# Performance work log

Hardware: AMD Instinct MI355X
Metric: run time of the kernel (lower is better)

## Reference

```python
import jax, jax.numpy as jnp
import numpy as np

NUM_HEADS = 12
HEAD_CH = 64
WINDOW = 4


def _relative_to_absolute(x):
    # x: (B, H, L, 2L-1) -> (B, H, L, L) via skew trick
    B, H, L, _ = x.shape
    x = jnp.pad(x, ((0, 0), (0, 0), (0, 0), (0, 1)))        # (B,H,L,2L)
    x = x.reshape(B, H, L * 2 * L)
    x = jnp.pad(x, ((0, 0), (0, 0), (0, L - 1)))
    x = x.reshape(B, H, L + 1, 2 * L - 1)
    return x[:, :, :L, L - 1:]


def _get_relative_embeddings(emb, L):
    # emb: (H, 2W+1, D) -> (H, 2L-1, D)
    pad = max(0, L - WINDOW - 1)
    start = max(0, WINDOW - L + 1)
    e = jnp.pad(emb, ((0, 0), (pad, pad), (0, 0)))
    return e[:, start:start + 2 * L - 1, :]


def _forward(x, wq, bq, wk, bk, wv, bv, wo, bo, emb_rel_k, emb_rel_v):
    B, C, L = x.shape
    H, D = NUM_HEADS, HEAD_CH
    scale = 1.0 / np.sqrt(D).astype(np.float32)

    # 1x1 conv == channel matmul
    q = jnp.einsum('oc,bcl->bol', wq, x) + bq[None, :, None]
    k = jnp.einsum('oc,bcl->bol', wk, x) + bk[None, :, None]
    v = jnp.einsum('oc,bcl->bol', wv, x) + bv[None, :, None]

    # (B, C, L) -> (B, H, L, D)
    q = q.reshape(B, H, D, L).transpose(0, 1, 3, 2)
    k = k.reshape(B, H, D, L).transpose(0, 1, 3, 2)
    v = v.reshape(B, H, D, L).transpose(0, 1, 3, 2)

    score = jnp.einsum('bhld,bhmd->bhlm', q, k) * scale      # (B,H,L,L)

    rel_k = _get_relative_embeddings(emb_rel_k, L)           # (H, 2L-1, D)
    s_rel = jnp.einsum('bhld,hmd->bhlm', q, rel_k)           # (B,H,L,2L-1)
    score = score + _relative_to_absolute(s_rel) * scale

    attn = jax.nn.softmax(score, axis=-1)                    # dropout p=0 -> identity

    res = jnp.einsum('bhlm,bhmd->bhld', attn, v)             # (B,H,L,D)

    # absolute_to_relative skew
    a = jnp.pad(attn, ((0, 0), (0, 0), (0, 0), (0, L - 1)))
    a = a.reshape(B, H, L * (2 * L - 1))
    a = jnp.pad(a, ((0, 0), (0, 0), (L, 0)))
    rel_w = a.reshape(B, H, L, 2 * L)[:, :, :, 1:]           # (B,H,L,2L-1)

    rel_v = _get_relative_embeddings(emb_rel_v, L)           # (H, 2L-1, D)
    res = res + jnp.einsum('bhlm,hmd->bhld', rel_w, rel_v)

    res = res.transpose(0, 1, 3, 2).reshape(B, H * D, L)     # (B, C, L)
    out = jnp.einsum('oc,bcl->bol', wo, res) + bo[None, :, None]
    return out


def setup_inputs() -> dict:
    key = jax.random.key(0)
    ks = jax.random.split(key, 11)
    B, C, L = 4, 768, 1024
    rel_std = HEAD_CH ** (-0.5)
    xavier = np.sqrt(6.0 / (C + C)).astype(np.float32)
    return {
        'x': jax.random.normal(ks[0], (B, C, L), jnp.float32),
        'wq': jax.random.uniform(ks[1], (C, C), jnp.float32, -xavier, xavier),
        'bq': jnp.zeros((C,), jnp.float32),
        'wk': jax.random.uniform(ks[2], (C, C), jnp.float32, -xavier, xavier),
        'bk': jnp.zeros((C,), jnp.float32),
        'wv': jax.random.uniform(ks[3], (C, C), jnp.float32, -xavier, xavier),
        'bv': jnp.zeros((C,), jnp.float32),
        'wo': jax.random.normal(ks[4], (C, C), jnp.float32) * 0.02,
        'bo': jnp.zeros((C,), jnp.float32),
        'emb_rel_k': jax.random.normal(ks[5], (NUM_HEADS, 2 * WINDOW + 1, HEAD_CH), jnp.float32) * rel_std,
        'emb_rel_v': jax.random.normal(ks[6], (NUM_HEADS, 2 * WINDOW + 1, HEAD_CH), jnp.float32) * rel_std,
    }


def reference(x, wq, bq, wk, bk, wv, bv, wo, bo, emb_rel_k, emb_rel_v):
    return _forward(x, wq, bq, wk, bk, wv, bv, wo, bo, emb_rel_k, emb_rel_v)
```

## Files before the change

kernel.cpp:

```cpp
#include <hip/hip_runtime.h>

#define NB   4
#define NH   12
#define HD   64
#define CCH  768
#define LQ   1024
#define SCALE 0.125f
#define STAB  4.0f
#define SC2  0.18033688f
#define ST2  5.7707802f
#define WELE (CCH*CCH)

typedef unsigned short u16;
typedef __bf16 bf16x8 __attribute__((ext_vector_type(8)));
typedef unsigned short u16x8 __attribute__((ext_vector_type(8)));
typedef unsigned short u16x4 __attribute__((ext_vector_type(4)));
typedef float floatx4 __attribute__((ext_vector_type(4)));

__device__ __forceinline__ float bf2f(u16 u) {
    union { unsigned int i; float f; } x; x.i = ((unsigned int)u) << 16; return x.f;
}
__device__ __forceinline__ u16 f2bf_u(float f) {
    union { float f; unsigned int i; } x; x.f = f;
    unsigned int i = x.i;
    return (u16)((i + 0x7FFFu + ((i >> 16) & 1u)) >> 16);
}
__device__ __forceinline__ void glds16(const u16* g, u16* l) {
    __builtin_amdgcn_global_load_lds(
        (const __attribute__((address_space(1))) unsigned int*)g,
        (__attribute__((address_space(3))) unsigned int*)l, 16, 0, 0);
}

__global__ __launch_bounds__(256) void convert_w_kernel(
    const float* __restrict__ wq, const float* __restrict__ wk,
    const float* __restrict__ wv, const float* __restrict__ wo,
    u16* __restrict__ wb)
{
    const int p = blockIdx.y;
    const float* src = (p == 0) ? wq : (p == 1) ? wk : (p == 2) ? wv : wo;
    u16* dst = wb + (size_t)p * WELE;
    const int idx = (blockIdx.x * 256 + threadIdx.x) * 4;
    const float4 v = *reinterpret_cast<const float4*>(src + idx);
    u16x4 o;
    o[0] = f2bf_u(v.x); o[1] = f2bf_u(v.y); o[2] = f2bf_u(v.z); o[3] = f2bf_u(v.w);
    *reinterpret_cast<u16x4*>(dst + idx) = o;
}

__global__ __launch_bounds__(256) void transpose_x_kernel(
    const float* __restrict__ x, u16* __restrict__ xT)
{
    __shared__ u16 tile[64 * 68];
    const int l0 = blockIdx.x * 64, c0 = blockIdx.y * 64, b = blockIdx.z;
    const int t = threadIdx.x;
    const float* xb = x + (size_t)b * CCH * LQ;
    {
        const int l = t & 63, cg = t >> 6;
        for (int i = 0; i < 16; ++i) {
            const int c = cg * 16 + i;
            tile[c * 68 + l] = f2bf_u(xb[(size_t)(c0 + c) * LQ + l0 + l]);
        }
    }
    __syncthreads();
    {
        const int c = t & 63, lg = t >> 6;
        for (int i = 0; i < 16; ++i) {
            const int l = lg * 16 + i;
            xT[((size_t)b * LQ + l0 + l) * CCH + c0 + c] = tile[c * 68 + l];
        }
    }
}

#define GEMM_CORE(Ag, Bg)                                                     \
    __shared__ __align__(16) u16 a_tile[128 * 64];                            \
    __shared__ __align__(16) u16 b_tile[128 * 64];                            \
    const int t = threadIdx.x;                                                \
    const int wave = t >> 6, lane = t & 63;                                   \
    const int quad = lane >> 4, l16 = lane & 15;                              \
    const int wm = (wave >> 1) * 64, wn = (wave & 1) * 64;                    \
    floatx4 acc[4][4];                                                        \
    _Pragma("unroll") for (int mi = 0; mi < 4; ++mi)                          \
        _Pragma("unroll") for (int ni = 0; ni < 4; ++ni)                      \
            _Pragma("unroll") for (int r = 0; r < 4; ++r) acc[mi][ni][r] = 0.f;\
    for (int k0 = 0; k0 < CCH; k0 += 64) {                                    \
        __syncthreads();                                                      \
        _Pragma("unroll") for (int i = 0; i < 4; ++i) {                       \
            const int sbase = wave * 256 + i * 64;                            \
            const int s = sbase + lane;                                       \
            const int m = s >> 3, pos = s & 7;                                \
            const int gpos = pos ^ (m & 7);                                   \
            glds16(Ag + (size_t)(m0 + m) * CCH + k0 + gpos * 8,               \
                   &a_tile[sbase * 8]);                                       \
            glds16(Bg + (size_t)(n0 + m) * CCH + k0 + gpos * 8,               \
                   &b_tile[sbase * 8]);                                       \
        }                                                                     \
        __syncthreads();                                                      \
        bf16x8 af[2][4], bfr[2][4];                                           \
        _Pragma("unroll") for (int s = 0; s < 2; ++s)                         \
            _Pragma("unroll") for (int i = 0; i < 4; ++i) {                   \
                const int am = wm + i * 16 + l16;                             \
                const int bn = wn + i * 16 + l16;                             \
                const int c = s * 4 + quad;                                   \
                af[s][i]  = *reinterpret_cast<const bf16x8*>(                 \
                    &a_tile[(am * 8 + (c ^ (am & 7))) * 8]);                  \
                bfr[s][i] = *reinterpret_cast<const bf16x8*>(                 \
                    &b_tile[(bn * 8 + (c ^ (bn & 7))) * 8]);                  \
            }                                                                 \
        _Pragma("unroll") for (int s = 0; s < 2; ++s)                         \
            _Pragma("unroll") for (int mi = 0; mi < 4; ++mi)                  \
                _Pragma("unroll") for (int ni = 0; ni < 4; ++ni)              \
                    acc[mi][ni] = __builtin_amdgcn_mfma_f32_16x16x32_bf16(    \
                        af[s][mi], bfr[s][ni], acc[mi][ni], 0, 0, 0);         \
    }

__global__ __launch_bounds__(256) void proj_qkv_kernel(
    const u16* __restrict__ xT, const u16* __restrict__ wb,
    const float* __restrict__ bq, const float* __restrict__ bk,
    const float* __restrict__ bv,
    u16* __restrict__ Qw, u16* __restrict__ Kw, u16* __restrict__ Vw)
{
    const int z = blockIdx.z, b = z / 3, p = z % 3;
    int m0, n0;
    const u16 *Ag, *Bg;
    if (p == 1) {
        m0 = blockIdx.x * 128;
        n0 = blockIdx.y * 128;
        Ag = xT + (size_t)b * LQ * CCH;
        Bg = wb + (size_t)WELE;
    } else {
        n0 = blockIdx.x * 128;
        m0 = blockIdx.y * 128;
        Ag = wb + (size_t)p * WELE;
        Bg = xT + (size_t)b * LQ * CCH;
    }

    GEMM_CORE(Ag, Bg)

    if (p == 1) {
        u16* Y = Kw + (size_t)b * LQ * CCH;
#pragma unroll
        for (int mi = 0; mi < 4; ++mi) {
#pragma unroll
            for (int r = 0; r < 4; ++r) {
                const int l = m0 + wm + mi * 16 + quad * 4 + r;
#pragma unroll
                for (int ni = 0; ni < 4; ++ni) {
                    const int o = n0 + wn + ni * 16 + l16;
                    Y[(size_t)l * CCH + o] = f2bf_u(acc[mi][ni][r] + bk[o]);
                }
            }
        }
    } else {
        const float* bias = (p == 0) ? bq : bv;
        u16* Y = ((p == 0) ? Qw : Vw) + (size_t)b * CCH * LQ;
#pragma unroll
        for (int mi = 0; mi < 4; ++mi) {
#pragma unroll
            for (int r = 0; r < 4; ++r) {
                const int o = m0 + wm + mi * 16 + quad * 4 + r;
                const float bb = bias[o];
#pragma unroll
                for (int ni = 0; ni < 4; ++ni) {
                    const int l = n0 + wn + ni * 16 + l16;
                    Y[(size_t)o * LQ + l] = f2bf_u(acc[mi][ni][r] + bb);
                }
            }
        }
    }
}

__global__ __launch_bounds__(256) void proj_out_kernel(
    const u16* __restrict__ resb, const u16* __restrict__ wb,
    const float* __restrict__ bo, float* __restrict__ out)
{
    const int b = blockIdx.z;
    const int n0 = blockIdx.x * 128, m0 = blockIdx.y * 128;
    const u16* Ag = wb + (size_t)3 * WELE;
    const u16* Bg = resb + (size_t)b * LQ * CCH;
    float* Y = out + (size_t)b * CCH * LQ;

    GEMM_CORE(Ag, Bg)

#pragma unroll
    for (int mi = 0; mi < 4; ++mi) {
#pragma unroll
        for (int r = 0; r < 4; ++r) {
            const int o = m0 + wm + mi * 16 + quad * 4 + r;
            const float bb = bo[o];
#pragma unroll
            for (int ni = 0; ni < 4; ++ni) {
                const int l = n0 + wn + ni * 16 + l16;
                Y[(size_t)o * LQ + l] = acc[mi][ni][r] + bb;
            }
        }
    }
}

#define KSTRIDE 72
#define TILE_E  (64 * 64)

__device__ __forceinline__ void stage_kv(
    const u16* __restrict__ Kb, const u16* __restrict__ Vb, int j0,
    u16* kb_lds, u16* vb_lds, int wave, int lane)
{
#pragma unroll
    for (int i = 0; i < 4; ++i) {
        const int sidx = wave * 4 + i;
        if (sidx < 8) {
            const int sbase = sidx * 64;
            const int s = sbase + lane;
            const int m = s >> 3, pos = s & 7;
            const int gpos = pos ^ (m & 7);
            glds16(Kb + (size_t)(j0 + m) * CCH + gpos * 8, &kb_lds[sbase * 8]);
        } else {
            const int sbase = (sidx - 8) * 64;
            const int s = sbase + lane;
            const int m = s >> 3, pos = s & 7;
            const int gpos = pos ^ (m & 7);
            glds16(Vb + (size_t)m * LQ + j0 + gpos * 8, &vb_lds[sbase * 8]);
        }
    }
}

__global__ __launch_bounds__(256) void attn_kernel(
    const u16* __restrict__ Qw, const u16* __restrict__ Kt,
    const u16* __restrict__ Vw,
    const float* __restrict__ erk, const float* __restrict__ erv,
    u16* __restrict__ resb)
{
    __shared__ __align__(16) u16 kbuf[2 * TILE_E];
    __shared__ __align__(16) u16 vbuf[2 * TILE_E];
    __shared__ __align__(16) u16 p_lds[4 * 16 * KSTRIDE];
    __shared__ float bias_lds[64 * 9];
    __shared__ float bandw_lds[64 * 9];
    __shared__ float erk_lds[9 * 64];
    __shared__ float erv_lds[9 * 64];

    const int t = threadIdx.x;
    const int wave = t >> 6, lane = t & 63;
    const int quad = lane >> 4, l16 = lane & 15;
    const int l0 = blockIdx.x * 64, h = blockIdx.y, b = blockIdx.z;
    const int rbase = wave * 16;
    const size_t base = ((size_t)b * CCH + (size_t)h * HD) * LQ;
    const u16* Qb = Qw + base;
    const u16* Vb = Vw + base;
    const u16* Kb = Kt + (size_t)b * LQ * CCH + (size_t)h * HD;

    for (int i = t; i < 9 * 64; i += 256) {
        erk_lds[i] = erk[(size_t)h * 9 * 64 + i];
        erv_lds[i] = erv[(size_t)h * 9 * 64 + i];
    }

    bf16x8 qa0, qa1;
    {
        const int lg = l0 + rbase + l16;
        union { u16x8 u; bf16x8 v; } t0, t1;
#pragma unroll
        for (int jj = 0; jj < 8; ++jj) {
            t0.u[jj] = Qb[(size_t)(quad * 8 + jj) * LQ + lg];
            t1.u[jj] = Qb[(size_t)(32 + quad * 8 + jj) * LQ + lg];
        }
        qa0 = t0.v; qa1 = t1.v;
    }

    stage_kv(Kb, Vb, 0, kbuf, vbuf, wave, lane);

    __syncthreads();

    {
        union { bf16x8 v; u16x8 u; } a0, a1; a0.v = qa0; a1.v = qa1;
        float qf[16];
#pragma unroll
        for (int jj = 0; jj < 8; ++jj) { qf[jj] = bf2f(a0.u[jj]); qf[8 + jj] = bf2f(a1.u[jj]); }
        for (int dl = 0; dl < 9; ++dl) {
            float s = 0.f;
#pragma unroll
            for (int jj = 0; jj < 8; ++jj) {
                s += qf[jj]     * erk_lds[dl * 64 + quad * 8 + jj];
                s += qf[8 + jj] * erk_lds[dl * 64 + 32 + quad * 8 + jj];
            }
            s += __shfl_xor(s, 16, 64);
            s += __shfl_xor(s, 32, 64);
            if (quad == 0) bias_lds[(rbase + l16) * 9 + dl] = s;
        }
    }

    floatx4 O[4];
    float l_acc = 0.f;
#pragma unroll
    for (int i = 0; i < 4; ++i)
#pragma unroll
        for (int r = 0; r < 4; ++r) O[i][r] = 0.f;

    u16* pw = p_lds + wave * 16 * KSTRIDE;
    const int qrow = rbase + l16;
    const int lgq = l0 + qrow;

    for (int kb = 0; kb < 16; ++kb) {
        const int j0 = kb * 64;
        __syncthreads();
        if (kb < 15)
            stage_kv(Kb, Vb, j0 + 64,
                     kbuf + ((kb + 1) & 1) * TILE_E,
                     vbuf + ((kb + 1) & 1) * TILE_E, wave, lane);
        const u16* kt = kbuf + (kb & 1) * TILE_E;
        const u16* vt = vbuf + (kb & 1) * TILE_E;

        floatx4 s4[4];
#pragma unroll
        for (int tt = 0; tt < 4; ++tt) {
            const int row = tt * 16 + l16;
            const bf16x8 ka0 = *reinterpret_cast<const bf16x8*>(
                &kt[(row * 8 + (quad ^ (row & 7))) * 8]);
            const bf16x8 ka1 = *reinterpret_cast<const bf16x8*>(
                &kt[(row * 8 + ((quad + 4) ^ (row & 7))) * 8]);
            floatx4 c;
#pragma unroll
            for (int r = 0; r < 4; ++r) c[r] = 0.f;
            c = __builtin_amdgcn_mfma_f32_16x16x32_bf16(ka0, qa0, c, 0, 0, 0);
            c = __builtin_amdgcn_mfma_f32_16x16x32_bf16(ka1, qa1, c, 0, 0, 0);
            s4[tt] = c;
        }

        {
            const int lgmin = l0 + rbase, lgmax = lgmin + 15;
            if (j0 + 63 >= lgmin - 4 && j0 <= lgmax + 4) {
#pragma unroll
                for (int tt = 0; tt < 4; ++tt) {
#pragma unroll
                    for (int r = 0; r < 4; ++r) {
                        const int key = j0 + tt * 16 + quad * 4 + r;
                        const int delta = key - lgq + 4;
                        if (delta >= 0 && delta <= 8) s4[tt][r] += bias_lds[qrow * 9 + delta];
                    }
                }
            }
        }

#pragma unroll
        for (int tt = 0; tt < 4; ++tt) {
            u16x4 pk;
#pragma unroll
            for (int r = 0; r < 4; ++r) {
                const float p = __builtin_amdgcn_exp2f(fmaf(s4[tt][r], SC2, -ST2));
                l_acc += p;
                pk[r] = f2bf_u(p);
            }
            *reinterpret_cast<u16x4*>(&pw[l16 * KSTRIDE + tt * 16 + quad * 4]) = pk;
        }

        const bf16x8 pa0 = *reinterpret_cast<const bf16x8*>(&pw[l16 * KSTRIDE + quad * 8]);
        const bf16x8 pa1 = *reinterpret_cast<const bf16x8*>(&pw[l16 * KSTRIDE + 32 + quad * 8]);
#pragma unroll
        for (int tt = 0; tt < 4; ++tt) {
            const int vrow = tt * 16 + l16;
            const bf16x8 vb0 = *reinterpret_cast<const bf16x8*>(
                &vt[(vrow * 8 + (quad ^ (vrow & 7))) * 8]);
            const bf16x8 vb1 = *reinterpret_cast<const bf16x8*>(
                &vt[(vrow * 8 + ((quad + 4) ^ (vrow & 7))) * 8]);
            O[tt] = __builtin_amdgcn_mfma_f32_16x16x32_bf16(pa0, vb0, O[tt], 0, 0, 0);
            O[tt] = __builtin_amdgcn_mfma_f32_16x16x32_bf16(pa1, vb1, O[tt], 0, 0, 0);
        }
    }

    float l_tot = l_acc;
    l_tot += __shfl_xor(l_tot, 16, 64);
    l_tot += __shfl_xor(l_tot, 32, 64);

    {
        union { bf16x8 v; u16x8 u; } a0, a1; a0.v = qa0; a1.v = qa1;
        float qf[16];
#pragma unroll
        for (int jj = 0; jj < 8; ++jj) { qf[jj] = bf2f(a0.u[jj]); qf[8 + jj] = bf2f(a1.u[jj]); }
        for (int dl = 0; dl < 9; ++dl) {
            const int jgl = lgq + dl - 4;
            const int jc = min(max(jgl, 0), LQ - 1);
            const u16* kr = Kb + (size_t)jc * CCH;
            union { bf16x8 v; u16x8 u; } k0, k1;
            k0.v = *reinterpret_cast<const bf16x8*>(kr + quad * 8);
            k1.v = *reinterpret_cast<const bf16x8*>(kr + 32 + quad * 8);
            float s = 0.f;
#pragma unroll
            for (int jj = 0; jj < 8; ++jj) {
                s += qf[jj]     * bf2f(k0.u[jj]);
                s += qf[8 + jj] * bf2f(k1.u[jj]);
            }
            s += __shfl_xor(s, 16, 64);
            s += __shfl_xor(s, 32, 64);
            float pband = 0.f;
            if (jgl >= 0 && jgl < LQ)
                pband = __builtin_amdgcn_exp2f(fmaf(s + bias_lds[qrow * 9 + dl], SC2, -ST2));
            if (quad == 0) bandw_lds[qrow * 9 + dl] = pband;
        }
    }

    float rinv[4];
#pragma unroll
    for (int r = 0; r < 4; ++r) {
        const int src = (lane & 48) | (quad * 4 + r);
        rinv[r] = 1.0f / __shfl(l_tot, src, 64);
    }

#pragma unroll
    for (int tt = 0; tt < 4; ++tt) {
#pragma unroll
        for (int r = 0; r < 4; ++r) {
            const int row = rbase + quad * 4 + r;
            const int d = tt * 16 + l16;
            float val = O[tt][r];
#pragma unroll
            for (int dl = 0; dl < 9; ++dl)
                val += bandw_lds[row * 9 + dl] * erv_lds[dl * 64 + d];
            val *= rinv[r];
            resb[((size_t)b * LQ + (l0 + row)) * CCH + h * HD + d] = f2bf_u(val);
        }
    }
}

extern "C" void kernel_launch(void* const* d_in, const int* in_sizes, int n_in,
                              void* d_out, int out_size, void* d_ws, size_t ws_size,
                              hipStream_t stream) {
    const float* x   = (const float*)d_in[0];
    const float* wq  = (const float*)d_in[1];
    const float* bq  = (const float*)d_in[2];
    const float* wk  = (const float*)d_in[3];
    const float* bk  = (const float*)d_in[4];
    const float* wv  = (const float*)d_in[5];
    const float* bv  = (const float*)d_in[6];
    const float* wo  = (const float*)d_in[7];
    const float* bo  = (const float*)d_in[8];
    const float* erk = (const float*)d_in[9];
    const float* erv = (const float*)d_in[10];
    float* out = (float*)d_out;

    const size_t NEL = (size_t)NB * CCH * LQ;
    u16* xT   = (u16*)d_ws;
    u16* wb   = xT + NEL;
    u16* Qw   = wb + (size_t)4 * WELE;
    u16* Kw   = Qw + NEL;
    u16* Vw   = Kw + NEL;
    u16* resb = Vw + NEL;

    convert_w_kernel<<<dim3(WELE / 1024, 4), 256, 0, stream>>>(wq, wk, wv, wo, wb);
    transpose_x_kernel<<<dim3(16, 12, 4), 256, 0, stream>>>(x, xT);
    proj_qkv_kernel<<<dim3(8, 6, 12), 256, 0, stream>>>(
        xT, wb, bq, bk, bv, Qw, Kw, Vw);
    attn_kernel<<<dim3(LQ / 64, NH, NB), 256, 0, stream>>>(
        Qw, Kw, Vw, erk, erv, resb);
    proj_out_kernel<<<dim3(8, 6, 4), 256, 0, stream>>>(resb, wb, bo, out);
}
```

Baseline: 189.5 us.

## Double-buffer GEMM LDS tiles and swizzle workgroups for XCD cache locality

```diff
diff --git a/kernel.cpp b/kernel.cpp
--- a/kernel.cpp
+++ b/kernel.cpp
@@ -70,9 +70,23 @@
     }
 }
 
+#define GEMM_STAGE(Ag, Bg, k0, abuf, bbuf)                                    \
+    {                                                                         \
+        _Pragma("unroll") for (int i = 0; i < 4; ++i) {                       \
+            const int sbase = wave * 256 + i * 64;                            \
+            const int s = sbase + lane;                                       \
+            const int m = s >> 3, pos = s & 7;                                \
+            const int gpos = pos ^ (m & 7);                                   \
+            glds16(Ag + (size_t)(m0 + m) * CCH + (k0) + gpos * 8,             \
+                   &(abuf)[sbase * 8]);                                       \
+            glds16(Bg + (size_t)(n0 + m) * CCH + (k0) + gpos * 8,             \
+                   &(bbuf)[sbase * 8]);                                       \
+        }                                                                     \
+    }
+
 #define GEMM_CORE(Ag, Bg)                                                     \
-    __shared__ __align__(16) u16 a_tile[128 * 64];                            \
-    __shared__ __align__(16) u16 b_tile[128 * 64];                            \
+    __shared__ __align__(16) u16 a_tile[2][128 * 64];                         \
+    __shared__ __align__(16) u16 b_tile[2][128 * 64];                         \
     const int t = threadIdx.x;                                                \
     const int wave = t >> 6, lane = t & 63;                                   \
     const int quad = lane >> 4, l16 = lane & 15;                              \
@@ -81,19 +95,14 @@
     _Pragma("unroll") for (int mi = 0; mi < 4; ++mi)                          \
         _Pragma("unroll") for (int ni = 0; ni < 4; ++ni)                      \
             _Pragma("unroll") for (int r = 0; r < 4; ++r) acc[mi][ni][r] = 0.f;\
-    for (int k0 = 0; k0 < CCH; k0 += 64) {                                    \
+    GEMM_STAGE(Ag, Bg, 0, a_tile[0], b_tile[0])                               \
+    for (int kk = 0; kk < CCH / 64; ++kk) {                                   \
         __syncthreads();                                                      \
-        _Pragma("unroll") for (int i = 0; i < 4; ++i) {                       \
-            const int sbase = wave * 256 + i * 64;                            \
-            const int s = sbase + lane;                                       \
-            const int m = s >> 3, pos = s & 7;                                \
-            const int gpos = pos ^ (m & 7);                                   \
-            glds16(Ag + (size_t)(m0 + m) * CCH + k0 + gpos * 8,               \
-                   &a_tile[sbase * 8]);                                       \
-            glds16(Bg + (size_t)(n0 + m) * CCH + k0 + gpos * 8,               \
-                   &b_tile[sbase * 8]);                                       \
-        }                                                                     \
-        __syncthreads();                                                      \
+        if (kk + 1 < CCH / 64)                                                \
+            GEMM_STAGE(Ag, Bg, (kk + 1) * 64,                                 \
+                       a_tile[(kk + 1) & 1], b_tile[(kk + 1) & 1])            \
+        const u16* at = a_tile[kk & 1];                                       \
+        const u16* bt = b_tile[kk & 1];                                       \
         bf16x8 af[2][4], bfr[2][4];                                           \
         _Pragma("unroll") for (int s = 0; s < 2; ++s)                         \
             _Pragma("unroll") for (int i = 0; i < 4; ++i) {                   \
@@ -101,9 +110,9 @@
                 const int bn = wn + i * 16 + l16;                             \
                 const int c = s * 4 + quad;                                   \
                 af[s][i]  = *reinterpret_cast<const bf16x8*>(                 \
-                    &a_tile[(am * 8 + (c ^ (am & 7))) * 8]);                  \
+                    &at[(am * 8 + (c ^ (am & 7))) * 8]);                      \
                 bfr[s][i] = *reinterpret_cast<const bf16x8*>(                 \
-                    &b_tile[(bn * 8 + (c ^ (bn & 7))) * 8]);                  \
+                    &bt[(bn * 8 + (c ^ (bn & 7))) * 8]);                      \
             }                                                                 \
         _Pragma("unroll") for (int s = 0; s < 2; ++s)                         \
             _Pragma("unroll") for (int mi = 0; mi < 4; ++mi)                  \
@@ -118,17 +127,21 @@
     const float* __restrict__ bv,
     u16* __restrict__ Qw, u16* __restrict__ Kw, u16* __restrict__ Vw)
 {
-    const int z = blockIdx.z, b = z / 3, p = z % 3;
+    const int wg0 = blockIdx.x + 8 * (blockIdx.y + 6 * blockIdx.z);
+    const int swz = (wg0 & 7) * 72 + (wg0 >> 3);
+    const int bx = swz % 8, rest = swz / 8;
+    const int by = rest % 6, z = rest / 6;
+    const int b = z / 3, p = z % 3;
     int m0, n0;
     const u16 *Ag, *Bg;
     if (p == 1) {
-        m0 = blockIdx.x * 128;
-        n0 = blockIdx.y * 128;
+        m0 = bx * 128;
+        n0 = by * 128;
         Ag = xT + (size_t)b * LQ * CCH;
         Bg = wb + (size_t)WELE;
     } else {
-        n0 = blockIdx.x * 128;
-        m0 = blockIdx.y * 128;
+        n0 = bx * 128;
+        m0 = by * 128;
         Ag = wb + (size_t)p * WELE;
         Bg = xT + (size_t)b * LQ * CCH;
     }
@@ -172,8 +185,11 @@
     const u16* __restrict__ resb, const u16* __restrict__ wb,
     const float* __restrict__ bo, float* __restrict__ out)
 {
-    const int b = blockIdx.z;
-    const int n0 = blockIdx.x * 128, m0 = blockIdx.y * 128;
+    const int wg0 = blockIdx.x + 8 * (blockIdx.y + 6 * blockIdx.z);
+    const int swz = (wg0 & 7) * 24 + (wg0 >> 3);
+    const int bx = swz % 8, rest = swz / 8;
+    const int by = rest % 6, b = rest / 6;
+    const int n0 = bx * 128, m0 = by * 128;
     const u16* Ag = wb + (size_t)3 * WELE;
     const u16* Bg = resb + (size_t)b * LQ * CCH;
     float* Y = out + (size_t)b * CCH * LQ;
@@ -238,7 +254,11 @@
     const int t = threadIdx.x;
     const int wave = t >> 6, lane = t & 63;
     const int quad = lane >> 4, l16 = lane & 15;
-    const int l0 = blockIdx.x * 64, h = blockIdx.y, b = blockIdx.z;
+    const int wg = blockIdx.x + 16 * (blockIdx.y + 12 * blockIdx.z);
+    const int rr = wg & 7, j = wg >> 3;
+    const int l0 = (j & 15) * 64;
+    const int hb = rr + 8 * (j >> 4);
+    const int h = hb % NH, b = hb / NH;
     const int rbase = wave * 16;
     const size_t base = ((size_t)b * CCH + (size_t)h * HD) * LQ;
     const u16* Qb = Qw + base;
```

New measurement: 187.0 us. No clear change (-1.3%).
